# Optimization experiments

Measured on AMD Instinct MI355X. Metric: run time of the kernel, lower is better.

Reference implementation:

```python
import jax, jax.numpy as jnp
import numpy as np

# dims: L=tgt len, S=src len, N=batch, E=embed, H=heads
L, S, N, E, H = 1024, 1024, 4, 1024, 16
HD = E // H  # head dim = 64


def setup_inputs() -> dict:
    key = jax.random.key(0)
    ks = jax.random.split(key, 7)
    w_scale = 0.02
    return {
        "query": jax.random.normal(ks[0], (L, N, E), jnp.float32),
        "key": jax.random.normal(ks[1], (S, N, E), jnp.float32),
        "value": jax.random.normal(ks[2], (S, N, E), jnp.float32),
        "in_proj_weight": jax.random.normal(ks[3], (3 * E, E), jnp.float32) * w_scale,
        "in_proj_bias": jax.random.normal(ks[4], (3 * E,), jnp.float32) * w_scale,
        "out_proj_weight": jax.random.normal(ks[5], (E, E), jnp.float32) * w_scale,
        "out_proj_bias": jax.random.normal(ks[6], (E,), jnp.float32) * w_scale,
    }


def reference(query, key, value, in_proj_weight, in_proj_bias,
              out_proj_weight, out_proj_bias):
    scaling = float(HD) ** -0.5
    # packed QKV projection, sliced exactly as the torch code does
    q = (query @ in_proj_weight[:E].T + in_proj_bias[:E]) * scaling        # (L,N,E)
    k = key @ in_proj_weight[E:2 * E].T + in_proj_bias[E:2 * E]            # (S,N,E)
    v = value @ in_proj_weight[2 * E:].T + in_proj_bias[2 * E:]            # (S,N,E)
    # split heads: (L,N,E) -> (N*H, L, HD)
    q = q.reshape(L, N * H, HD).transpose(1, 0, 2)
    k = k.reshape(S, N * H, HD).transpose(1, 0, 2)
    v = v.reshape(S, N * H, HD).transpose(1, 0, 2)
    scores = jnp.einsum('bld,bsd->bls', q, k)          # (N*H, L, S)
    attn = jax.nn.softmax(scores, axis=-1)
    sig = jax.nn.sigmoid(scores)                        # the need_sigmoid_weights variant
    out = jnp.einsum('bls,bsd->bld', attn, v)          # (N*H, L, HD)
    out = out.transpose(1, 0, 2).reshape(L, N, E)
    out = out @ out_proj_weight.T + out_proj_bias       # (L,N,E)
    # weights averaged over heads, as torch MHA returns: (N,L,S)
    attn_weights = attn.reshape(N, H, L, S).sum(axis=1) / H
    sig_weights = sig.reshape(N, H, L, S).sum(axis=1) / H
    return out, attn_weights, sig_weights
```

## Files before the change

kernel.cpp:

```cpp
#include <hip/hip_runtime.h>

#define L_DIM 1024
#define E_DIM 1024
#define NB 4
#define H_NUM 16
#define HD_DIM 64
#define T_TOK 4096
#define NHB 64

typedef float f32x4 __attribute__((ext_vector_type(4)));
typedef unsigned short u16x8 __attribute__((ext_vector_type(8)));
typedef unsigned short u16x4 __attribute__((ext_vector_type(4)));
typedef __bf16 bf16x8 __attribute__((ext_vector_type(8)));

__device__ inline unsigned short f2bf(float f) {
  unsigned int u = __builtin_bit_cast(unsigned int, f);
  u += 0x7FFFu + ((u >> 16) & 1u);
  return (unsigned short)(u >> 16);
}
__device__ __forceinline__ unsigned int cvt_pk_bf16(float lo, float hi) {
  unsigned int r;
  asm("v_cvt_pk_bf16_f32 %0, %1, %2" : "=v"(r) : "v"(lo), "v"(hi));
  return r;
}
__device__ inline f32x4 mfma16(u16x8 a, u16x8 b, f32x4 c) {
  return __builtin_amdgcn_mfma_f32_16x16x32_bf16(
      __builtin_bit_cast(bf16x8, a), __builtin_bit_cast(bf16x8, b), c, 0, 0, 0);
}

__device__ __forceinline__ void gl2lds16(const void* g, void* l) {
  auto gp = reinterpret_cast<const __attribute__((address_space(1))) unsigned int*>(
      reinterpret_cast<unsigned long long>(g));
  auto lp = reinterpret_cast<__attribute__((address_space(3))) unsigned int*>(
      static_cast<unsigned int>(reinterpret_cast<unsigned long long>(l)));
  __builtin_amdgcn_global_load_lds(gp, lp, 16, 0, 0);
}

__global__ __launch_bounds__(256) void cast_kernel(
    const float* __restrict__ s0, const float* __restrict__ s1,
    const float* __restrict__ s2, const float* __restrict__ s3,
    const float* __restrict__ s4,
    unsigned short* __restrict__ d0, unsigned short* __restrict__ d1,
    unsigned short* __restrict__ d2, unsigned short* __restrict__ d3,
    unsigned short* __restrict__ d4,
    int n0, int n1, int n2, int n3, int n4) {
  const int y = blockIdx.y;
  const float* s = (y == 0) ? s0 : (y == 1) ? s1 : (y == 2) ? s2 : (y == 3) ? s3 : s4;
  unsigned short* d = (y == 0) ? d0 : (y == 1) ? d1 : (y == 2) ? d2 : (y == 3) ? d3 : d4;
  const int n = (y == 0) ? n0 : (y == 1) ? n1 : (y == 2) ? n2 : (y == 3) ? n3 : n4;
  int idx = (blockIdx.x * 256 + threadIdx.x) * 8;
  const int stride = gridDim.x * 256 * 8;
  for (; idx < n; idx += stride) {
    float4 a = *(const float4*)(s + idx);
    float4 b = *(const float4*)(s + idx + 4);
    u16x8 o = {f2bf(a.x), f2bf(a.y), f2bf(a.z), f2bf(a.w),
               f2bf(b.x), f2bf(b.y), f2bf(b.z), f2bf(b.w)};
    *(u16x8*)(d + idx) = o;
  }
}

__device__ __forceinline__ void stage_tile(const unsigned short* __restrict__ g,
                                           unsigned short* lbuf, int tid) {
  const int r = tid >> 2, c = tid & 3;
  const int sc = c ^ ((r ^ (r >> 2)) & 3);
  gl2lds16(g + (size_t)r * 1024 + sc * 8, lbuf + tid * 8);
  const int r2 = r + 64;
  gl2lds16(g + (size_t)r2 * 1024 + sc * 8, lbuf + (tid + 256) * 8);
}
__device__ __forceinline__ int frag_off(int r, int q) {
  return r * 32 + ((q ^ ((r ^ (r >> 2)) & 3)) << 3);
}

__global__ __launch_bounds__(256) void qkv_gemm(
    const unsigned short* __restrict__ qb, const unsigned short* __restrict__ kb,
    const unsigned short* __restrict__ vb, const unsigned short* __restrict__ Wb,
    const float* __restrict__ bias, unsigned short* __restrict__ q_hm,
    unsigned short* __restrict__ k_hm, unsigned short* __restrict__ v_t) {
  __shared__ __align__(16) unsigned short As[3][4096];
  __shared__ __align__(16) unsigned short Bs[3][4096];
  const int tid = threadIdx.x;
  const int bm = blockIdx.x, bn = blockIdx.y, z = blockIdx.z;
  const unsigned short* Ag = ((z == 0) ? qb : (z == 1) ? kb : vb) + (size_t)bm * 128 * 1024;
  const unsigned short* Bg = Wb + (size_t)z * 1048576 + (size_t)bn * 128 * 1024;
  const float* bc = bias + z * E_DIM;

  const int w = tid >> 6, lane = tid & 63;
  const int wm = w & 1, wn = w >> 1;
  const int quad = lane >> 4, l16 = lane & 15;

  f32x4 acc[4][4];
#pragma unroll
  for (int i = 0; i < 4; i++)
#pragma unroll
    for (int j = 0; j < 4; j++) { f32x4 zz = {0.f, 0.f, 0.f, 0.f}; acc[i][j] = zz; }

  stage_tile(Ag, As[0], tid);
  stage_tile(Bg, Bs[0], tid);

  int cb = 0, sb = 1;
#pragma unroll 1
  for (int kk = 0; kk < 32; kk++) {
    if (kk + 1 < 32) {
      stage_tile(Ag + (kk + 1) * 32, As[sb], tid);
      stage_tile(Bg + (kk + 1) * 32, Bs[sb], tid);
      sb = (sb == 2) ? 0 : sb + 1;
      asm volatile("s_waitcnt vmcnt(4)" ::: "memory");
    } else {
      asm volatile("s_waitcnt vmcnt(0)" ::: "memory");
    }
    __builtin_amdgcn_s_barrier();
    asm volatile("" ::: "memory");
    u16x8 af[4], bfv[4];
#pragma unroll
    for (int mi = 0; mi < 4; mi++) {
      int r = wm * 64 + mi * 16 + l16;
      af[mi] = *(const u16x8*)&As[cb][frag_off(r, quad)];
    }
#pragma unroll
    for (int ni = 0; ni < 4; ni++) {
      int r = wn * 64 + ni * 16 + l16;
      bfv[ni] = *(const u16x8*)&Bs[cb][frag_off(r, quad)];
    }
#pragma unroll
    for (int mi = 0; mi < 4; mi++)
#pragma unroll
      for (int ni = 0; ni < 4; ni++)
        acc[mi][ni] = mfma16(af[mi], bfv[ni], acc[mi][ni]);
    cb = (cb == 2) ? 0 : cb + 1;
  }
#pragma unroll
  for (int ni = 0; ni < 4; ni++) {
    int col = bn * 128 + wn * 64 + ni * 16 + l16;
    float bv = bc[col];
    int h = col >> 6, d = col & 63;
#pragma unroll
    for (int mi = 0; mi < 4; mi++) {
#pragma unroll
      for (int r = 0; r < 4; r++) {
        int t = bm * 128 + wm * 64 + mi * 16 + quad * 4 + r;
        float v = acc[mi][ni][r] + bv;
        int nb = t & 3, pos = t >> 2;
        if (z == 0) {
          v *= 0.125f;
          q_hm[(size_t)((nb * 16 + h) * 1024 + pos) * 64 + d] = f2bf(v);
        } else if (z == 1) {
          k_hm[(size_t)((nb * 16 + h) * 1024 + pos) * 64 + d] = f2bf(v);
        } else {
          v_t[(size_t)((nb * 16 + h) * 64 + d) * 1024 + pos] = f2bf(v);
        }
      }
    }
  }
}

__global__ __launch_bounds__(256, 2) void attn_kernel(
    const unsigned short* __restrict__ q_hm, const unsigned short* __restrict__ k_hm,
    const unsigned short* __restrict__ v_t, unsigned short* __restrict__ o_h,
    float* __restrict__ m_ws, float* __restrict__ r_ws) {
  __shared__ __align__(16) unsigned short stage[6][4096];
  __shared__ __align__(16) unsigned short pt[4][32][68];
  __shared__ float red_m[4][32];
  __shared__ float red_s[4][32];

  const int tid = threadIdx.x;
  const int flat = blockIdx.x + (blockIdx.y << 5);
  const int nf = (flat & 7) * 256 + (flat >> 3);
  const int l0 = (nf & 31) * 32;
  const int b = nf >> 5;
  const int nb = b >> 4, h = b & 15;
  const int w = tid >> 6, lane = tid & 63;
  const int quad = lane >> 4, l16 = lane & 15;

  const int i1 = tid + 256;
  const int r0s = tid >> 3, c0s = tid & 7;
  const int r1s = i1 >> 3, c1s = i1 & 7;
  const int src0 = (c0s ^ (r0s & 7)) * 8;
  const int src1 = (c1s ^ (r1s & 7)) * 8;

  const unsigned short* kbase = k_hm + ((size_t)b << 16);
  const unsigned short* vbase = v_t + ((size_t)b << 16);

  u16x8 bq[2][2];
#pragma unroll
  for (int g = 0; g < 2; g++) {
    const unsigned short* qp =
        q_hm + ((size_t)(b * 1024 + l0 + g * 16 + l16) << 6) + quad * 8;
    bq[g][0] = *(const u16x8*)qp;
    bq[g][1] = *(const u16x8*)(qp + 32);
  }
  asm volatile("" ::: "memory");

  f32x4 acc[16][2];
#pragma unroll
  for (int j = 0; j < 16; j++)
#pragma unroll
    for (int g = 0; g < 2; g++) { f32x4 z = {0.f, 0.f, 0.f, 0.f}; acc[j][g] = z; }

#pragma unroll
  for (int t = 0; t < 4; t++) {
    gl2lds16(kbase + ((size_t)(t * 64 + r0s) << 6) + src0, &stage[t][tid * 8]);
    gl2lds16(kbase + ((size_t)(t * 64 + r1s) << 6) + src1, &stage[t][i1 * 8]);
  }

  const int myrow = w * 16 + l16;
  const int sw0 = ((quad ^ (l16 & 7)) * 8);
  const int sw1 = (((quad + 4) ^ (l16 & 7)) * 8);

#pragma unroll
  for (int i = 0; i < 8; i++) {
    if (i >= 1) {
      const int t0 = 2 * i + 2, t1 = 2 * i + 3;
      if (t0 < 16) {
        gl2lds16(kbase + ((size_t)(t0 * 64 + r0s) << 6) + src0, &stage[t0 % 6][tid * 8]);
        gl2lds16(kbase + ((size_t)(t0 * 64 + r1s) << 6) + src1, &stage[t0 % 6][i1 * 8]);
        gl2lds16(kbase + ((size_t)(t1 * 64 + r0s) << 6) + src0, &stage[t1 % 6][tid * 8]);
        gl2lds16(kbase + ((size_t)(t1 * 64 + r1s) << 6) + src1, &stage[t1 % 6][i1 * 8]);
      } else {
        const int v0 = t0 - 16, v1 = t1 - 16;
        gl2lds16(vbase + ((size_t)r0s << 10) + v0 * 64 + src0, &stage[t0 % 6][tid * 8]);
        gl2lds16(vbase + ((size_t)r1s << 10) + v0 * 64 + src1, &stage[t0 % 6][i1 * 8]);
        gl2lds16(vbase + ((size_t)r0s << 10) + v1 * 64 + src0, &stage[t1 % 6][tid * 8]);
        gl2lds16(vbase + ((size_t)r1s << 10) + v1 * 64 + src1, &stage[t1 % 6][i1 * 8]);
      }
    }
    asm volatile("s_waitcnt vmcnt(4)" ::: "memory");
    __builtin_amdgcn_s_barrier();
    asm volatile("" ::: "memory");
    const int c0 = 2 * i, c1 = 2 * i + 1;
    const unsigned short* kt0 = &stage[c0 % 6][myrow * 64];
    const unsigned short* kt1 = &stage[c1 % 6][myrow * 64];
    u16x8 a00 = *(const u16x8*)(kt0 + sw0);
    u16x8 a01 = *(const u16x8*)(kt0 + sw1);
    u16x8 a10 = *(const u16x8*)(kt1 + sw0);
    u16x8 a11 = *(const u16x8*)(kt1 + sw1);
    acc[c0][0] = mfma16(a00, bq[0][0], acc[c0][0]);
    acc[c0][0] = mfma16(a01, bq[0][1], acc[c0][0]);
    acc[c0][1] = mfma16(a00, bq[1][0], acc[c0][1]);
    acc[c0][1] = mfma16(a01, bq[1][1], acc[c0][1]);
    acc[c1][0] = mfma16(a10, bq[0][0], acc[c1][0]);
    acc[c1][0] = mfma16(a11, bq[0][1], acc[c1][0]);
    acc[c1][1] = mfma16(a10, bq[1][0], acc[c1][1]);
    acc[c1][1] = mfma16(a11, bq[1][1], acc[c1][1]);
  }

  gl2lds16(vbase + ((size_t)r0s << 10) + 2 * 64 + src0, &stage[0][tid * 8]);
  gl2lds16(vbase + ((size_t)r1s << 10) + 2 * 64 + src1, &stage[0][i1 * 8]);
  gl2lds16(vbase + ((size_t)r0s << 10) + 3 * 64 + src0, &stage[1][tid * 8]);
  gl2lds16(vbase + ((size_t)r1s << 10) + 3 * 64 + src1, &stage[1][i1 * 8]);

  float lm0 = -3e38f, lm1 = -3e38f;
#pragma unroll
  for (int j = 0; j < 16; j++)
#pragma unroll
    for (int r = 0; r < 4; r++) {
      lm0 = fmaxf(lm0, acc[j][0][r]);
      lm1 = fmaxf(lm1, acc[j][1][r]);
    }
  lm0 = fmaxf(lm0, __shfl_xor(lm0, 16, 64));
  lm0 = fmaxf(lm0, __shfl_xor(lm0, 32, 64));
  lm1 = fmaxf(lm1, __shfl_xor(lm1, 16, 64));
  lm1 = fmaxf(lm1, __shfl_xor(lm1, 32, 64));
  if (lane < 16) { red_m[w][lane] = lm0; red_m[w][lane + 16] = lm1; }
  asm volatile("s_waitcnt lgkmcnt(0)" ::: "memory");
  __builtin_amdgcn_s_barrier();
  asm volatile("" ::: "memory");
  float m0 = fmaxf(fmaxf(red_m[0][l16], red_m[1][l16]),
                   fmaxf(red_m[2][l16], red_m[3][l16]));
  float m1 = fmaxf(fmaxf(red_m[0][l16 + 16], red_m[1][l16 + 16]),
                   fmaxf(red_m[2][l16 + 16], red_m[3][l16 + 16]));
  float mm = 0.f;
  if (tid < 32)
    mm = fmaxf(fmaxf(red_m[0][tid], red_m[1][tid]),
               fmaxf(red_m[2][tid], red_m[3][tid]));

  float ls0 = 0.f, ls1 = 0.f;
  auto exppk = [&](int t, int slot) {
    float e0a = __expf(acc[t][0][0] - m0), e0b = __expf(acc[t][0][1] - m0);
    float e0c = __expf(acc[t][0][2] - m0), e0d = __expf(acc[t][0][3] - m0);
    float e1a = __expf(acc[t][1][0] - m1), e1b = __expf(acc[t][1][1] - m1);
    float e1c = __expf(acc[t][1][2] - m1), e1d = __expf(acc[t][1][3] - m1);
    ls0 += (e0a + e0b) + (e0c + e0d);
    ls1 += (e1a + e1b) + (e1c + e1d);
    uint2 p0 = {cvt_pk_bf16(e0a, e0b), cvt_pk_bf16(e0c, e0d)};
    uint2 p1 = {cvt_pk_bf16(e1a, e1b), cvt_pk_bf16(e1c, e1d)};
    *(uint2*)&pt[slot][l16][w * 16 + quad * 4] = p0;
    *(uint2*)&pt[slot][16 + l16][w * 16 + quad * 4] = p1;
  };
  exppk(0, 0);
  exppk(1, 1);

  f32x4 oacc0 = {0.f, 0.f, 0.f, 0.f};
  f32x4 oacc1 = {0.f, 0.f, 0.f, 0.f};
#pragma unroll
  for (int i = 0; i < 8; i++) {
    if (i >= 1 && i <= 6) {
      const int v0 = 2 * i + 2, v1 = 2 * i + 3;
      const int b0 = (v0 + 16) % 6, b1 = (v1 + 16) % 6;
      gl2lds16(vbase + ((size_t)r0s << 10) + v0 * 64 + src0, &stage[b0][tid * 8]);
      gl2lds16(vbase + ((size_t)r1s << 10) + v0 * 64 + src1, &stage[b0][i1 * 8]);
      gl2lds16(vbase + ((size_t)r0s << 10) + v1 * 64 + src0, &stage[b1][tid * 8]);
      gl2lds16(vbase + ((size_t)r1s << 10) + v1 * 64 + src1, &stage[b1][i1 * 8]);
    }
    if (i < 7) {
      asm volatile("s_waitcnt vmcnt(4) lgkmcnt(0)" ::: "memory");
    } else {
      asm volatile("s_waitcnt vmcnt(0) lgkmcnt(0)" ::: "memory");
    }
    __builtin_amdgcn_s_barrier();
    asm volatile("" ::: "memory");
    if (i < 7) {
      exppk(2 * i + 2, (2 * i + 2) % 4);
      exppk(2 * i + 3, (2 * i + 3) % 4);
    }
    const int cA = 2 * i, cB = 2 * i + 1;
    const unsigned short* vt0 = &stage[(cA + 16) % 6][myrow * 64];
    const unsigned short* vt1 = &stage[(cB + 16) % 6][myrow * 64];
    u16x8 bvA0 = *(const u16x8*)(vt0 + sw0);
    u16x8 bvA1 = *(const u16x8*)(vt0 + sw1);
    u16x8 bvB0 = *(const u16x8*)(vt1 + sw0);
    u16x8 bvB1 = *(const u16x8*)(vt1 + sw1);
    u16x8 apA00 = *(const u16x8*)&pt[cA % 4][l16][quad * 8];
    u16x8 apA01 = *(const u16x8*)&pt[cA % 4][l16][32 + quad * 8];
    u16x8 apA10 = *(const u16x8*)&pt[cA % 4][16 + l16][quad * 8];
    u16x8 apA11 = *(const u16x8*)&pt[cA % 4][16 + l16][32 + quad * 8];
    u16x8 apB00 = *(const u16x8*)&pt[cB % 4][l16][quad * 8];
    u16x8 apB01 = *(const u16x8*)&pt[cB % 4][l16][32 + quad * 8];
    u16x8 apB10 = *(const u16x8*)&pt[cB % 4][16 + l16][quad * 8];
    u16x8 apB11 = *(const u16x8*)&pt[cB % 4][16 + l16][32 + quad * 8];
    oacc0 = mfma16(apA00, bvA0, oacc0);
    oacc0 = mfma16(apA01, bvA1, oacc0);
    oacc0 = mfma16(apB00, bvB0, oacc0);
    oacc0 = mfma16(apB01, bvB1, oacc0);
    oacc1 = mfma16(apA10, bvA0, oacc1);
    oacc1 = mfma16(apA11, bvA1, oacc1);
    oacc1 = mfma16(apB10, bvB0, oacc1);
    oacc1 = mfma16(apB11, bvB1, oacc1);
  }

  ls0 += __shfl_xor(ls0, 16, 64);
  ls0 += __shfl_xor(ls0, 32, 64);
  ls1 += __shfl_xor(ls1, 16, 64);
  ls1 += __shfl_xor(ls1, 32, 64);
  if (lane < 16) { red_s[w][lane] = ls0; red_s[w][lane + 16] = ls1; }
  asm volatile("s_waitcnt lgkmcnt(0)" ::: "memory");
  __builtin_amdgcn_s_barrier();
  asm volatile("" ::: "memory");
  float rv0 = 1.0f / (red_s[0][l16] + red_s[1][l16] + red_s[2][l16] + red_s[3][l16]);
  float rv1 = 1.0f / (red_s[0][l16 + 16] + red_s[1][l16 + 16] +
                      red_s[2][l16 + 16] + red_s[3][l16 + 16]);
  if (tid < 32) {
    float ssv = red_s[0][tid] + red_s[1][tid] + red_s[2][tid] + red_s[3][tid];
    m_ws[b * 1024 + l0 + tid] = mm;
    r_ws[b * 1024 + l0 + tid] = 1.0f / ssv;
  }

#pragma unroll
  for (int r = 0; r < 4; r++) {
    int lr = quad * 4 + r;
    float rr0 = __shfl(rv0, lr, 64);
    float rr1 = __shfl(rv1, lr, 64);
    int t0 = (l0 + lr) * 4 + nb;
    int t1 = (l0 + 16 + lr) * 4 + nb;
    o_h[((size_t)t0 << 10) + h * 64 + w * 16 + l16] = f2bf(oacc0[r] * rr0);
    o_h[((size_t)t1 << 10) + h * 64 + w * 16 + l16] = f2bf(oacc1[r] * rr1);
  }
}

__global__ __launch_bounds__(256, 2) void weights_kernel(
    const unsigned short* __restrict__ q_hm, const unsigned short* __restrict__ k_hm,
    const float* __restrict__ m_ws, const float* __restrict__ r_ws,
    float* __restrict__ attn_out, float* __restrict__ sig_out) {
  __shared__ __align__(16) unsigned short qs[4][4096];
  __shared__ __align__(16) unsigned short ks[4][4096];
  __shared__ float ml[16][64];
  __shared__ float rl[16][64];
  __shared__ float cl[16][64];

  const int tid = threadIdx.x;
  const int flat = blockIdx.x + (blockIdx.y << 4) + (blockIdx.z << 8);
  const int xcd = flat & 7, local = flat >> 3;
  const int nb = xcd >> 1;
  const int idx2 = ((xcd & 1) << 7) + local;
  const int l0 = (idx2 >> 4) << 6;
  const int s0 = (idx2 & 15) << 6;

  const int w = tid >> 6, lane = tid & 63;
  const int quad = lane >> 4, l16 = lane & 15;

  const int i1 = tid + 256;
  const int r0s = tid >> 3, c0s = tid & 7;
  const int r1s = i1 >> 3, c1s = i1 & 7;
  const int src0 = (c0s ^ (r0s & 7)) * 8;
  const int src1 = (c1s ^ (r1s & 7)) * 8;

  {
    int idx = tid * 4;
    int hh = idx >> 6, ii = idx & 63;
    int bb = nb * 16 + hh;
    float4 mv4 = *(const float4*)&m_ws[bb * 1024 + l0 + ii];
    float4 rv4 = *(const float4*)&r_ws[bb * 1024 + l0 + ii];
    *(float4*)&ml[hh][ii] = mv4;
    *(float4*)&rl[hh][ii] = rv4;
    float4 cv4 = {__expf(-mv4.x), __expf(-mv4.y), __expf(-mv4.z), __expf(-mv4.w)};
    *(float4*)&cl[hh][ii] = cv4;
  }

  const int sw0 = ((quad ^ (l16 & 7)) * 8);
  const int sw1 = (((quad + 4) ^ (l16 & 7)) * 8);

  auto stageQK = [&](int h) {
    const int bb = nb * 16 + h;
    const unsigned short* qb = q_hm + ((size_t)(bb * 1024 + l0) << 6);
    const unsigned short* kb = k_hm + ((size_t)(bb * 1024 + s0) << 6);
    const int bf = h & 3;
    gl2lds16(qb + (r0s << 6) + src0, &qs[bf][tid * 8]);
    gl2lds16(qb + (r1s << 6) + src1, &qs[bf][i1 * 8]);
    gl2lds16(kb + (r0s << 6) + src0, &ks[bf][tid * 8]);
    gl2lds16(kb + (r1s << 6) + src1, &ks[bf][i1 * 8]);
  };

  f32x4 accA[4], accS[4];
#pragma unroll
  for (int i = 0; i < 4; i++) {
    f32x4 zz = {0.f, 0.f, 0.f, 0.f};
    accA[i] = zz; accS[i] = zz;
  }

  stageQK(0);
  stageQK(1);
  asm volatile("s_waitcnt lgkmcnt(0)" ::: "memory");

  auto computeH = [&](int h) {
    const int bf = h & 3;
    const unsigned short* qt = &qs[bf][(w * 16 + l16) * 64];
    u16x8 a0 = *(const u16x8*)(qt + sw0);
    u16x8 a1 = *(const u16x8*)(qt + sw1);
    f32x4 mv = *(const f32x4*)&ml[h][w * 16 + quad * 4];
    f32x4 rv = *(const f32x4*)&rl[h][w * 16 + quad * 4];
    f32x4 cv = *(const f32x4*)&cl[h][w * 16 + quad * 4];
#pragma unroll
    for (int ni = 0; ni < 4; ni++) {
      const unsigned short* kt = &ks[bf][(ni * 16 + l16) * 64];
      u16x8 b0 = *(const u16x8*)(kt + sw0);
      u16x8 b1 = *(const u16x8*)(kt + sw1);
      f32x4 scv = {0.f, 0.f, 0.f, 0.f};
      scv = mfma16(a0, b0, scv);
      scv = mfma16(a1, b1, scv);
#pragma unroll
      for (int r = 0; r < 4; r++) {
        float e = __expf(scv[r] - mv[r]);
        accA[ni][r] += e * rv[r];
        accS[ni][r] += e * __builtin_amdgcn_rcpf(e + cv[r]);
      }
    }
  };

#pragma unroll 1
  for (int h = 0; h < 14; ++h) {
    stageQK(h + 2);
    asm volatile("s_waitcnt vmcnt(8)" ::: "memory");
    __builtin_amdgcn_s_barrier();
    asm volatile("" ::: "memory");
    computeH(h);
  }
  asm volatile("s_waitcnt vmcnt(4)" ::: "memory");
  __builtin_amdgcn_s_barrier();
  asm volatile("" ::: "memory");
  computeH(14);
  asm volatile("s_waitcnt vmcnt(0)" ::: "memory");
  __builtin_amdgcn_s_barrier();
  asm volatile("" ::: "memory");
  computeH(15);

  const float inv_h = 1.0f / 16.0f;
  const int lrow0 = l0 + w * 16;
#pragma unroll
  for (int ni = 0; ni < 4; ni++) {
#pragma unroll
    for (int r = 0; r < 4; r++) {
      int l = lrow0 + quad * 4 + r;
      int s = s0 + ni * 16 + l16;
      size_t idx = ((size_t)nb * 1024 + l) * 1024 + s;
      attn_out[idx] = accA[ni][r] * inv_h;
      sig_out[idx] = accS[ni][r] * inv_h;
    }
  }
}

__global__ __launch_bounds__(256) void out_gemm(
    const unsigned short* __restrict__ o_h, const unsigned short* __restrict__ Wb,
    const float* __restrict__ bias, float* __restrict__ out) {
  __shared__ __align__(16) unsigned short As[3][4096];
  __shared__ __align__(16) unsigned short Bs[3][4096];
  const int tid = threadIdx.x;
  const int bm = blockIdx.x, bn = blockIdx.y;
  const unsigned short* Ag = o_h + (size_t)bm * 128 * 1024;
  const unsigned short* Bg = Wb + (size_t)bn * 128 * 1024;

  const int w = tid >> 6, lane = tid & 63;
  const int wm = w & 1, wn = w >> 1;
  const int quad = lane >> 4, l16 = lane & 15;

  f32x4 acc[4][4];
#pragma unroll
  for (int i = 0; i < 4; i++)
#pragma unroll
    for (int j = 0; j < 4; j++) { f32x4 zz = {0.f, 0.f, 0.f, 0.f}; acc[i][j] = zz; }

  stage_tile(Ag, As[0], tid);
  stage_tile(Bg, Bs[0], tid);

  int cb = 0, sb = 1;
#pragma unroll 1
  for (int kk = 0; kk < 32; kk++) {
    if (kk + 1 < 32) {
      stage_tile(Ag + (kk + 1) * 32, As[sb], tid);
      stage_tile(Bg + (kk + 1) * 32, Bs[sb], tid);
      sb = (sb == 2) ? 0 : sb + 1;
      asm volatile("s_waitcnt vmcnt(4)" ::: "memory");
    } else {
      asm volatile("s_waitcnt vmcnt(0)" ::: "memory");
    }
    __builtin_amdgcn_s_barrier();
    asm volatile("" ::: "memory");
    u16x8 af[4], bfv[4];
#pragma unroll
    for (int mi = 0; mi < 4; mi++) {
      int r = wm * 64 + mi * 16 + l16;
      af[mi] = *(const u16x8*)&As[cb][frag_off(r, quad)];
    }
#pragma unroll
    for (int ni = 0; ni < 4; ni++) {
      int r = wn * 64 + ni * 16 + l16;
      bfv[ni] = *(const u16x8*)&Bs[cb][frag_off(r, quad)];
    }
#pragma unroll
    for (int mi = 0; mi < 4; mi++)
#pragma unroll
      for (int ni = 0; ni < 4; ni++)
        acc[mi][ni] = mfma16(af[mi], bfv[ni], acc[mi][ni]);
    cb = (cb == 2) ? 0 : cb + 1;
  }
#pragma unroll
  for (int ni = 0; ni < 4; ni++) {
    int col = bn * 128 + wn * 64 + ni * 16 + l16;
    float bv = bias[col];
#pragma unroll
    for (int mi = 0; mi < 4; mi++) {
#pragma unroll
      for (int r = 0; r < 4; r++) {
        int t = bm * 128 + wm * 64 + mi * 16 + quad * 4 + r;
        out[(size_t)t * E_DIM + col] = acc[mi][ni][r] + bv;
      }
    }
  }
}

extern "C" void kernel_launch(void* const* d_in, const int* in_sizes, int n_in,
                              void* d_out, int out_size, void* d_ws, size_t ws_size,
                              hipStream_t stream) {
  const float* qin  = (const float*)d_in[0];
  const float* kin  = (const float*)d_in[1];
  const float* vin  = (const float*)d_in[2];
  const float* Wqkv = (const float*)d_in[3];
  const float* bqkv = (const float*)d_in[4];
  const float* Wout = (const float*)d_in[5];
  const float* bout = (const float*)d_in[6];
  float* out      = (float*)d_out;
  float* attn_out = out + 4194304;
  float* sig_out  = out + 8388608;

  unsigned short* q_hm = (unsigned short*)d_ws;
  unsigned short* k_hm = q_hm + 4194304;
  unsigned short* v_t  = q_hm + 8388608;
  unsigned short* o_h  = q_hm + 12582912;
  float* m_ws = (float*)(q_hm + 16777216);
  float* r_ws = m_ws + 65536;

  unsigned short* qb = (unsigned short*)(out + 4194304);
  unsigned short* kb = qb + 4194304;
  unsigned short* vb = qb + 8388608;
  unsigned short* Wqkvb = o_h;
  unsigned short* Woutb = qb + 12582912;

  cast_kernel<<<dim3(2048, 5), 256, 0, stream>>>(
      qin, kin, vin, Wqkv, Wout, qb, kb, vb, Wqkvb, Woutb,
      4194304, 4194304, 4194304, 3145728, 1048576);
  qkv_gemm<<<dim3(32, 8, 3), 256, 0, stream>>>(qb, kb, vb, Wqkvb, bqkv,
                                               q_hm, k_hm, v_t);
  attn_kernel<<<dim3(32, 64), 256, 0, stream>>>(q_hm, k_hm, v_t, o_h, m_ws, r_ws);
  out_gemm<<<dim3(32, 8), 256, 0, stream>>>(o_h, Woutb, bout, out);
  weights_kernel<<<dim3(16, 16, 4), 256, 0, stream>>>(q_hm, k_hm, m_ws, r_ws,
                                                      attn_out, sig_out);
}
```

Before: 248.2 us.

## Load K fragments directly from global memory instead of LDS staging pipeline

Replaces the multi-buffered LDS staging pipeline for K in the QK^T phase with direct per-wave global loads of the K rows each wave needs. V prefetch now starts after the row-max reduction, and its buffer indices are simplified. This removes barriers and LDS traffic from the score loop. In exchange, global loads are uncoalesced, with 16-byte strided accesses, and K/V load overlap is lost. The custom barriers are also replaced with __syncthreads.

```diff
diff --git a/kernel.cpp b/kernel.cpp
--- a/kernel.cpp
+++ b/kernel.cpp
@@ -188,65 +188,27 @@
     bq[g][0] = *(const u16x8*)qp;
     bq[g][1] = *(const u16x8*)(qp + 32);
   }
-  asm volatile("" ::: "memory");
 
   f32x4 acc[16][2];
 #pragma unroll
   for (int j = 0; j < 16; j++)
 #pragma unroll
     for (int g = 0; g < 2; g++) { f32x4 z = {0.f, 0.f, 0.f, 0.f}; acc[j][g] = z; }
-
-#pragma unroll
-  for (int t = 0; t < 4; t++) {
-    gl2lds16(kbase + ((size_t)(t * 64 + r0s) << 6) + src0, &stage[t][tid * 8]);
-    gl2lds16(kbase + ((size_t)(t * 64 + r1s) << 6) + src1, &stage[t][i1 * 8]);
-  }
 
   const int myrow = w * 16 + l16;
   const int sw0 = ((quad ^ (l16 & 7)) * 8);
   const int sw1 = (((quad + 4) ^ (l16 & 7)) * 8);
 
 #pragma unroll
-  for (int i = 0; i < 8; i++) {
-    if (i >= 1) {
-      const int t0 = 2 * i + 2, t1 = 2 * i + 3;
-      if (t0 < 16) {
-        gl2lds16(kbase + ((size_t)(t0 * 64 + r0s) << 6) + src0, &stage[t0 % 6][tid * 8]);
-        gl2lds16(kbase + ((size_t)(t0 * 64 + r1s) << 6) + src1, &stage[t0 % 6][i1 * 8]);
-        gl2lds16(kbase + ((size_t)(t1 * 64 + r0s) << 6) + src0, &stage[t1 % 6][tid * 8]);
-        gl2lds16(kbase + ((size_t)(t1 * 64 + r1s) << 6) + src1, &stage[t1 % 6][i1 * 8]);
-      } else {
-        const int v0 = t0 - 16, v1 = t1 - 16;
-        gl2lds16(vbase + ((size_t)r0s << 10) + v0 * 64 + src0, &stage[t0 % 6][tid * 8]);
-        gl2lds16(vbase + ((size_t)r1s << 10) + v0 * 64 + src1, &stage[t0 % 6][i1 * 8]);
-        gl2lds16(vbase + ((size_t)r0s << 10) + v1 * 64 + src0, &stage[t1 % 6][tid * 8]);
-        gl2lds16(vbase + ((size_t)r1s << 10) + v1 * 64 + src1, &stage[t1 % 6][i1 * 8]);
-      }
-    }
-    asm volatile("s_waitcnt vmcnt(4)" ::: "memory");
-    __builtin_amdgcn_s_barrier();
-    asm volatile("" ::: "memory");
-    const int c0 = 2 * i, c1 = 2 * i + 1;
-    const unsigned short* kt0 = &stage[c0 % 6][myrow * 64];
-    const unsigned short* kt1 = &stage[c1 % 6][myrow * 64];
-    u16x8 a00 = *(const u16x8*)(kt0 + sw0);
-    u16x8 a01 = *(const u16x8*)(kt0 + sw1);
-    u16x8 a10 = *(const u16x8*)(kt1 + sw0);
-    u16x8 a11 = *(const u16x8*)(kt1 + sw1);
-    acc[c0][0] = mfma16(a00, bq[0][0], acc[c0][0]);
-    acc[c0][0] = mfma16(a01, bq[0][1], acc[c0][0]);
-    acc[c0][1] = mfma16(a00, bq[1][0], acc[c0][1]);
-    acc[c0][1] = mfma16(a01, bq[1][1], acc[c0][1]);
-    acc[c1][0] = mfma16(a10, bq[0][0], acc[c1][0]);
-    acc[c1][0] = mfma16(a11, bq[0][1], acc[c1][0]);
-    acc[c1][1] = mfma16(a10, bq[1][0], acc[c1][1]);
-    acc[c1][1] = mfma16(a11, bq[1][1], acc[c1][1]);
-  }
-
-  gl2lds16(vbase + ((size_t)r0s << 10) + 2 * 64 + src0, &stage[0][tid * 8]);
-  gl2lds16(vbase + ((size_t)r1s << 10) + 2 * 64 + src1, &stage[0][i1 * 8]);
-  gl2lds16(vbase + ((size_t)r0s << 10) + 3 * 64 + src0, &stage[1][tid * 8]);
-  gl2lds16(vbase + ((size_t)r1s << 10) + 3 * 64 + src1, &stage[1][i1 * 8]);
+  for (int j = 0; j < 16; j++) {
+    const unsigned short* kr = kbase + ((size_t)(j * 64 + myrow) << 6) + quad * 8;
+    u16x8 a0 = *(const u16x8*)kr;
+    u16x8 a1 = *(const u16x8*)(kr + 32);
+    acc[j][0] = mfma16(a0, bq[0][0], acc[j][0]);
+    acc[j][0] = mfma16(a1, bq[0][1], acc[j][0]);
+    acc[j][1] = mfma16(a0, bq[1][0], acc[j][1]);
+    acc[j][1] = mfma16(a1, bq[1][1], acc[j][1]);
+  }
 
   float lm0 = -3e38f, lm1 = -3e38f;
 #pragma unroll
@@ -261,9 +223,7 @@
   lm1 = fmaxf(lm1, __shfl_xor(lm1, 16, 64));
   lm1 = fmaxf(lm1, __shfl_xor(lm1, 32, 64));
   if (lane < 16) { red_m[w][lane] = lm0; red_m[w][lane + 16] = lm1; }
-  asm volatile("s_waitcnt lgkmcnt(0)" ::: "memory");
-  __builtin_amdgcn_s_barrier();
-  asm volatile("" ::: "memory");
+  __syncthreads();
   float m0 = fmaxf(fmaxf(red_m[0][l16], red_m[1][l16]),
                    fmaxf(red_m[2][l16], red_m[3][l16]));
   float m1 = fmaxf(fmaxf(red_m[0][l16 + 16], red_m[1][l16 + 16]),
@@ -272,6 +232,12 @@
   if (tid < 32)
     mm = fmaxf(fmaxf(red_m[0][tid], red_m[1][tid]),
                fmaxf(red_m[2][tid], red_m[3][tid]));
+
+#pragma unroll
+  for (int t = 0; t < 4; t++) {
+    gl2lds16(vbase + ((size_t)r0s << 10) + t * 64 + src0, &stage[t][tid * 8]);
+    gl2lds16(vbase + ((size_t)r1s << 10) + t * 64 + src1, &stage[t][i1 * 8]);
+  }
 
   float ls0 = 0.f, ls1 = 0.f;
   auto exppk = [&](int t, int slot) {
@@ -295,11 +261,10 @@
   for (int i = 0; i < 8; i++) {
     if (i >= 1 && i <= 6) {
       const int v0 = 2 * i + 2, v1 = 2 * i + 3;
-      const int b0 = (v0 + 16) % 6, b1 = (v1 + 16) % 6;
-      gl2lds16(vbase + ((size_t)r0s << 10) + v0 * 64 + src0, &stage[b0][tid * 8]);
-      gl2lds16(vbase + ((size_t)r1s << 10) + v0 * 64 + src1, &stage[b0][i1 * 8]);
-      gl2lds16(vbase + ((size_t)r0s << 10) + v1 * 64 + src0, &stage[b1][tid * 8]);
-      gl2lds16(vbase + ((size_t)r1s << 10) + v1 * 64 + src1, &stage[b1][i1 * 8]);
+      gl2lds16(vbase + ((size_t)r0s << 10) + v0 * 64 + src0, &stage[v0 % 6][tid * 8]);
+      gl2lds16(vbase + ((size_t)r1s << 10) + v0 * 64 + src1, &stage[v0 % 6][i1 * 8]);
+      gl2lds16(vbase + ((size_t)r0s << 10) + v1 * 64 + src0, &stage[v1 % 6][tid * 8]);
+      gl2lds16(vbase + ((size_t)r1s << 10) + v1 * 64 + src1, &stage[v1 % 6][i1 * 8]);
     }
     if (i < 7) {
       asm volatile("s_waitcnt vmcnt(4) lgkmcnt(0)" ::: "memory");
@@ -313,8 +278,8 @@
       exppk(2 * i + 3, (2 * i + 3) % 4);
     }
     const int cA = 2 * i, cB = 2 * i + 1;
-    const unsigned short* vt0 = &stage[(cA + 16) % 6][myrow * 64];
-    const unsigned short* vt1 = &stage[(cB + 16) % 6][myrow * 64];
+    const unsigned short* vt0 = &stage[cA % 6][myrow * 64];
+    const unsigned short* vt1 = &stage[cB % 6][myrow * 64];
     u16x8 bvA0 = *(const u16x8*)(vt0 + sw0);
     u16x8 bvA1 = *(const u16x8*)(vt0 + sw1);
     u16x8 bvB0 = *(const u16x8*)(vt1 + sw0);
@@ -342,9 +307,7 @@
   ls1 += __shfl_xor(ls1, 16, 64);
   ls1 += __shfl_xor(ls1, 32, 64);
   if (lane < 16) { red_s[w][lane] = ls0; red_s[w][lane + 16] = ls1; }
-  asm volatile("s_waitcnt lgkmcnt(0)" ::: "memory");
-  __builtin_amdgcn_s_barrier();
-  asm volatile("" ::: "memory");
+  __syncthreads();
   float rv0 = 1.0f / (red_s[0][l16] + red_s[1][l16] + red_s[2][l16] + red_s[3][l16]);
   float rv1 = 1.0f / (red_s[0][l16 + 16] + red_s[1][l16 + 16] +
                       red_s[2][l16 + 16] + red_s[3][l16 + 16]);
```

Result: slower. 262.5 us (+5.7%).
